# Kernel tuning notes

Hardware: AMD Instinct MI355X
Metric: run time of the kernel (lower is better)

## Reference

```python
import jax, jax.numpy as jnp
import numpy as np

B, C_IN, N = 32, 64, 128
OUT_FEATS = (64, 64, 128)
ATT_DIM = 64
EPS = 1e-5  # torch BatchNorm default


def _bn(x, g, b, m, v):
    # eval-mode BatchNorm over channel axis 1 (running stats m, v)
    shape = (1, -1) + (1,) * (x.ndim - 2)
    inv = g / jnp.sqrt(v + EPS)
    return (x - m.reshape(shape)) * inv.reshape(shape) + b.reshape(shape)


def setup_inputs() -> dict:
    key = jax.random.key(0)
    ks = iter(jax.random.split(key, 48))

    def w(shape, scale=0.05):
        return jax.random.normal(next(ks), shape, jnp.float32) * scale

    inp = {"features": jax.random.normal(next(ks), (B, C_IN, N), jnp.float32)}
    in_dims = (2 * C_IN, OUT_FEATS[0], OUT_FEATS[1])
    for li in range(3):
        o, ci = OUT_FEATS[li], in_dims[li]
        inp[f"w{li}"] = w((o, ci))                  # Conv2d 1x1, no bias (BN)
        inp[f"g{li}"] = 1.0 + w((o,))               # BN gamma
        inp[f"b{li}"] = w((o,))                     # BN beta
        inp[f"m{li}"] = w((o,))                     # BN running mean
        inp[f"v{li}"] = 1.0 + 0.1 * jax.random.uniform(next(ks), (o,), jnp.float32)
    inp["wa0"] = w((ATT_DIM, OUT_FEATS[-1]))        # attention conv (no bias)
    inp["ga"] = 1.0 + w((ATT_DIM,))
    inp["ba"] = w((ATT_DIM,))
    inp["ma"] = w((ATT_DIM,))
    inp["va"] = 1.0 + 0.1 * jax.random.uniform(next(ks), (ATT_DIM,), jnp.float32)
    inp["wa1"] = w((1, ATT_DIM))                    # final attention conv (bias)
    inp["ba1"] = w((1,))
    inp["wsc"] = w((OUT_FEATS[-1], C_IN))           # shortcut Conv1d (no bias)
    inp["gsc"] = 1.0 + w((OUT_FEATS[-1],))
    inp["bsc"] = w((OUT_FEATS[-1],))
    inp["msc"] = w((OUT_FEATS[-1],))
    inp["vsc"] = 1.0 + 0.1 * jax.random.uniform(next(ks), (OUT_FEATS[-1],), jnp.float32)
    return inp


def reference(features, w0, g0, b0, m0, v0, w1, g1, b1, m1, v1,
              w2, g2, b2, m2, v2, wa0, ga, ba, ma, va, wa1, ba1,
              wsc, gsc, bsc, msc, vsc):
    n = features.shape[-1]
    # neighbor index table: row i lists all j != i, shape (N, N-1)
    base = jnp.broadcast_to(jnp.arange(n)[None, :], (n, n))
    idx = jnp.where(base >= jnp.arange(n)[:, None], base + 1, base)[:, :-1]
    x_i = features[:, :, :, None]                   # (B,C,N,1)
    x_j = features[:, :, idx]                       # (B,C,N,N-1) gather
    x = jnp.concatenate([jnp.broadcast_to(x_i, x_j.shape), x_j - x_i], axis=1)  # (B,2C,N,N-1)
    for w_, g_, b_, m_, v_ in ((w0, g0, b0, m0, v0), (w1, g1, b1, m1, v1), (w2, g2, b2, m2, v2)):
        x = jnp.einsum('oc,bcnk->bonk', w_, x)      # 1x1 conv
        x = jax.nn.relu(_bn(x, g_, b_, m_, v_))
    # attention pooling over neighbor axis k
    a = jax.nn.relu(_bn(jnp.einsum('oc,bcnk->bonk', wa0, x), ga, ba, ma, va))
    logits = jnp.einsum('oc,bcnk->bonk', wa1, a) + ba1.reshape(1, 1, 1, 1)
    attw = jax.nn.softmax(logits[:, 0], axis=-1)    # (B,N,N-1)
    fts = jnp.einsum('bcnk,bnk->bcn', x, attw)      # (B,C_out,N)
    # shortcut branch (in_feat != out_feats[-1])
    sc = _bn(jnp.einsum('oc,bcn->bon', wsc, features), gsc, bsc, msc, vsc)
    return jax.nn.relu(sc + fts)
```

## Files before the change

kernel.cpp:

```cpp
#include <hip/hip_runtime.h>

typedef unsigned short u16;
typedef short short8 __attribute__((ext_vector_type(8)));
typedef float floatx4 __attribute__((ext_vector_type(4)));
typedef __bf16 bf16x2 __attribute__((ext_vector_type(2)));

#define MFMA16(a, b, c) __builtin_amdgcn_mfma_f32_16x16x32_bf16((a), (b), (c), 0, 0, 0)

#define W1F_OFF   0u
#define B1F_OFF   8192u
#define W2F_OFF   8448u
#define B2F_OFF   24832u
#define WA0F_OFF  25344u
#define BAF_OFF   41728u
#define WA1F_OFF  41984u
#define BA1F_OFF  42240u
#define P_OFF     42496u
#define Q_OFF     1091072u
#define SC_OFF    2139648u
#define WS_TOTAL  4236800u

__device__ __align__(256) char g_ws[WS_TOTAL];

#define LD0 72
#define LD2 136

__device__ __forceinline__ float bits2f(unsigned u) {
  union { unsigned i; float f; } v; v.i = u; return v.f;
}
__device__ __forceinline__ unsigned f2bits(float f) {
  union { float f; unsigned i; } v; v.f = f; return v.i;
}
__device__ __forceinline__ u16 f2bf(float f) {
  return (u16)((f2bits(f) + 0x8000u) >> 16);
}
__device__ __forceinline__ unsigned pack2relu(float a, float b) {
#if __has_builtin(__builtin_amdgcn_cvt_pk_bf16_f32)
  union { bf16x2 h; unsigned u; } cv;
  cv.h = __builtin_amdgcn_cvt_pk_bf16_f32(fmaxf(a, 0.f), fmaxf(b, 0.f));
  return cv.u;
#else
  unsigned lo = (f2bits(fmaxf(a, 0.f)) + 0x8000u) >> 16;
  unsigned hi = (f2bits(fmaxf(b, 0.f)) + 0x8000u) & 0xffff0000u;
  return lo | hi;
#endif
}

__global__ __launch_bounds__(256) void k_pre(
    const float* __restrict__ feat, const float* __restrict__ w0,
    const float* __restrict__ g0, const float* __restrict__ b0, const float* __restrict__ m0, const float* __restrict__ v0,
    const float* __restrict__ w1, const float* __restrict__ g1, const float* __restrict__ b1, const float* __restrict__ m1, const float* __restrict__ v1,
    const float* __restrict__ w2, const float* __restrict__ g2, const float* __restrict__ b2, const float* __restrict__ m2, const float* __restrict__ v2,
    const float* __restrict__ wa0, const float* __restrict__ ga, const float* __restrict__ ba, const float* __restrict__ ma, const float* __restrict__ va,
    const float* __restrict__ wa1, const float* __restrict__ ba1,
    const float* __restrict__ wsc, const float* __restrict__ gsc, const float* __restrict__ bsc, const float* __restrict__ msc, const float* __restrict__ vsc)
{
  __shared__ float smem[9600];
  const int t = threadIdx.x;
  char* ws = g_ws;
  const int blk = blockIdx.x;

  if (blk == 512) {
    float* fs1 = smem; float* fs2 = smem + 64; float* fsa = smem + 192;
    if (t < 64) {
      float s;
      s = g1[t] * rsqrtf(v1[t] + 1e-5f); fs1[t] = s; ((float*)(ws + B1F_OFF))[t] = b1[t] - m1[t] * s;
      s = ga[t] * rsqrtf(va[t] + 1e-5f); fsa[t] = s; ((float*)(ws + BAF_OFF))[t] = ba[t] - ma[t] * s;
      ((float*)(ws + WA1F_OFF))[t] = wa1[t];
    }
    if (t < 128) { float s = g2[t] * rsqrtf(v2[t] + 1e-5f); fs2[t] = s; ((float*)(ws + B2F_OFF))[t] = b2[t] - m2[t] * s; }
    if (t == 0) ((float*)(ws + BA1F_OFF))[0] = ba1[0];
    __syncthreads();
    u16* W1f = (u16*)(ws + W1F_OFF);
    u16* W2f = (u16*)(ws + W2F_OFF);
    u16* Wa0f = (u16*)(ws + WA0F_OFF);
    for (int i = t; i < 4096; i += 256) W1f[i]  = f2bf(fs1[i >> 6] * w1[i]);
    for (int i = t; i < 8192; i += 256) W2f[i]  = f2bf(fs2[i >> 6] * w2[i]);
    for (int i = t; i < 8192; i += 256) Wa0f[i] = f2bf(fsa[i >> 7] * wa0[i]);
    return;
  }

  const int sub = blk & 255;
  const int b = sub >> 3, n0 = (sub & 7) << 4;
  float* Xs  = smem;
  float* Wsm = smem + 1280;

  {
    const int c = t >> 2, j = (t & 3) << 2;
    *(float4*)(Xs + c * 20 + j) = *(const float4*)(feat + b * 8192 + c * 128 + n0 + j);
  }

  if (blk < 256) {
    #pragma unroll
    for (int r = 0; r < 8; r++) {
      const int i = (r * 256 + t) * 4;
      float4 v = *(const float4*)(w0 + i);
      const int o = i >> 7, c = i & 127;
      float* d = Wsm + o * 129 + c;
      d[0] = v.x; d[1] = v.y; d[2] = v.z; d[3] = v.w;
    }
    __syncthreads();
    const int o = t & 63, nb = (t >> 6) << 2;
    const float s  = g0[o] * rsqrtf(v0[o] + 1e-5f);
    const float tt = b0[o] - m0[o] * s;
    const float* wr = Wsm + o * 129;
    float dA0=0.f,dA1=0.f,dA2=0.f,dA3=0.f,dB0=0.f,dB1=0.f,dB2=0.f,dB3=0.f;
    #pragma unroll
    for (int c = 0; c < 64; c++) {
      const float a = wr[c], e = wr[64 + c];
      const float4 x = *(const float4*)(Xs + c * 20 + nb);
      dA0 += a * x.x; dA1 += a * x.y; dA2 += a * x.z; dA3 += a * x.w;
      dB0 += e * x.x; dB1 += e * x.y; dB2 += e * x.z; dB3 += e * x.w;
    }
    float* Pp = (float*)(ws + P_OFF) + (b * 128 + n0 + nb) * 64 + o;
    float* Qp = (float*)(ws + Q_OFF) + (b * 128 + n0 + nb) * 64 + o;
    Pp[0]   = s * dB0; Pp[64]  = s * dB1; Pp[128] = s * dB2; Pp[192] = s * dB3;
    Qp[0]   = s * (dA0 - dB0) + tt; Qp[64]  = s * (dA1 - dB1) + tt;
    Qp[128] = s * (dA2 - dB2) + tt; Qp[192] = s * (dA3 - dB3) + tt;
  } else {
    #pragma unroll
    for (int r = 0; r < 8; r++) {
      const int i = (r * 256 + t) * 4;
      float4 v = *(const float4*)(wsc + i);
      const int o = i >> 6, c = i & 63;
      float* d = Wsm + o * 65 + c;
      d[0] = v.x; d[1] = v.y; d[2] = v.z; d[3] = v.w;
    }
    __syncthreads();
    const int o = t & 127, h = (t >> 7) << 3;
    const float s  = gsc[o] * rsqrtf(vsc[o] + 1e-5f);
    const float tt = bsc[o] - msc[o] * s;
    const float* wr = Wsm + o * 65;
    float d0=0.f,d1=0.f,d2=0.f,d3=0.f,d4=0.f,d5=0.f,d6=0.f,d7=0.f;
    #pragma unroll
    for (int c = 0; c < 64; c++) {
      const float a = wr[c];
      const float4 x0 = *(const float4*)(Xs + c * 20 + h);
      const float4 x1 = *(const float4*)(Xs + c * 20 + h + 4);
      d0 += a * x0.x; d1 += a * x0.y; d2 += a * x0.z; d3 += a * x0.w;
      d4 += a * x1.x; d5 += a * x1.y; d6 += a * x1.z; d7 += a * x1.w;
    }
    float* SCp = (float*)(ws + SC_OFF) + (b * 128 + n0 + h) * 128 + o;
    SCp[0]   = s * d0 + tt; SCp[128] = s * d1 + tt; SCp[256] = s * d2 + tt; SCp[384] = s * d3 + tt;
    SCp[512] = s * d4 + tt; SCp[640] = s * d5 + tt; SCp[768] = s * d6 + tt; SCp[896] = s * d7 + tt;
  }
}

__global__ __launch_bounds__(256, 4) void k_main(float* __restrict__ out)
{
  __shared__ alignas(16) u16 buf[18432];
  __shared__ float parts[4][128];
  __shared__ float attws[128];

  const int blk = blockIdx.x, b = blk >> 7, n = blk & 127, t = threadIdx.x;
  const char* ws = g_ws;
  const float* Pb  = (const float*)(ws + P_OFF);
  const float* Qb  = (const float*)(ws + Q_OFF);
  const float* SCb = (const float*)(ws + SC_OFF);
  const u16*   W1f = (const u16*)(ws + W1F_OFF);
  const float* b1f = (const float*)(ws + B1F_OFF);
  const u16*   W2f = (const u16*)(ws + W2F_OFF);
  const float* b2f = (const float*)(ws + B2F_OFF);
  const u16*   Wa0f= (const u16*)(ws + WA0F_OFF);
  const float* baf = (const float*)(ws + BAF_OFF);
  const float* wa1f= (const float*)(ws + WA1F_OFF);
  const float  ba1v= *(const float*)(ws + BA1F_OFF);

  u16* H0 = buf;
  u16* H1 = buf + 9216;
  u16* H2 = buf;

  const int lane = t & 63, wid = t >> 6, quad = lane >> 4, l16 = lane & 15;
  const int koff = quad * 8;

  const short8 a1w0 = *(const short8*)(W1f + (wid * 16 + l16) * 64 + koff);
  const short8 a1w1 = *(const short8*)(W1f + (wid * 16 + l16) * 64 + 32 + koff);
  const short8 a2w00 = *(const short8*)(W2f + (wid * 32 + l16) * 64 + koff);
  const short8 a2w01 = *(const short8*)(W2f + (wid * 32 + l16) * 64 + 32 + koff);
  const short8 a2w10 = *(const short8*)(W2f + (wid * 32 + 16 + l16) * 64 + koff);
  const short8 a2w11 = *(const short8*)(W2f + (wid * 32 + 16 + l16) * 64 + 32 + koff);

  {
    const int k = t >> 1, half = t & 1;
    const int j = (k < 127) ? ((k < n) ? k : (k + 1)) : n;
    const float4* pr = (const float4*)(Pb + ((b << 7) + j) * 64 + half * 32);
    const float4* qr = (const float4*)(Qb + blk * 64 + half * 32);
    u16* dst = H0 + k * LD0 + half * 32;
    #pragma unroll
    for (int i = 0; i < 8; i++) {
      float4 p = pr[i], q = qr[i];
      uint2 sv;
      sv.x = pack2relu(q.x + p.x, q.y + p.y);
      sv.y = pack2relu(q.z + p.z, q.w + p.w);
      *(uint2*)(dst + i * 4) = sv;
    }
  }
  __syncthreads();

  {
    const int rr = wid * 16 + quad * 4;
    const float4 bb = *(const float4*)(b1f + rr);
    floatx4 binit; binit[0] = bb.x; binit[1] = bb.y; binit[2] = bb.z; binit[3] = bb.w;
    floatx4 acc[8];
    #pragma unroll
    for (int et = 0; et < 8; et++) acc[et] = binit;
    #pragma unroll
    for (int et = 0; et < 8; et++) {
      const u16* br = H0 + (et * 16 + l16) * LD0 + koff;
      short8 bf0 = *(const short8*)(br);
      short8 bf1 = *(const short8*)(br + 32);
      acc[et] = MFMA16(a1w0, bf0, acc[et]);
      acc[et] = MFMA16(a1w1, bf1, acc[et]);
    }
    #pragma unroll
    for (int et = 0; et < 8; et++) {
      uint2 sv;
      sv.x = pack2relu(acc[et][0], acc[et][1]);
      sv.y = pack2relu(acc[et][2], acc[et][3]);
      *(uint2*)(H1 + (et * 16 + l16) * LD0 + rr) = sv;
    }
  }
  __syncthreads();

  {
    const int r2 = wid * 32 + quad * 4;
    const float4 bba = *(const float4*)(b2f + r2);
    const float4 bbb = *(const float4*)(b2f + r2 + 16);
    floatx4 ia; ia[0] = bba.x; ia[1] = bba.y; ia[2] = bba.z; ia[3] = bba.w;
    floatx4 ib; ib[0] = bbb.x; ib[1] = bbb.y; ib[2] = bbb.z; ib[3] = bbb.w;
    floatx4 acc[2][8];
    #pragma unroll
    for (int et = 0; et < 8; et++) { acc[0][et] = ia; acc[1][et] = ib; }
    #pragma unroll
    for (int et = 0; et < 8; et++) {
      const u16* br = H1 + (et * 16 + l16) * LD0 + koff;
      short8 bf0 = *(const short8*)(br);
      short8 bf1 = *(const short8*)(br + 32);
      acc[0][et] = MFMA16(a2w00, bf0, acc[0][et]);
      acc[0][et] = MFMA16(a2w01, bf1, acc[0][et]);
      acc[1][et] = MFMA16(a2w10, bf0, acc[1][et]);
      acc[1][et] = MFMA16(a2w11, bf1, acc[1][et]);
    }
    __syncthreads();
    #pragma unroll
    for (int m = 0; m < 2; m++) {
      const int rr = r2 + m * 16;
      #pragma unroll
      for (int et = 0; et < 8; et++) {
        uint2 sv;
        sv.x = pack2relu(acc[m][et][0], acc[m][et][1]);
        sv.y = pack2relu(acc[m][et][2], acc[m][et][3]);
        *(uint2*)(H2 + (et * 16 + l16) * LD2 + rr) = sv;
      }
    }
  }
  __syncthreads();

  float scv = 0.f;
  if (t < 128) scv = SCb[blk * 128 + t];
  float* outp = out + ((b << 7) + (t & 127)) * 128 + n;

  {
    short8 a3[4];
    #pragma unroll
    for (int ks = 0; ks < 4; ks++)
      a3[ks] = *(const short8*)(Wa0f + (wid * 16 + l16) * 128 + ks * 32 + koff);
    const int rr = wid * 16 + quad * 4;
    const float4 bb = *(const float4*)(baf + rr);
    const float4 wv = *(const float4*)(wa1f + rr);
    floatx4 binit; binit[0] = bb.x; binit[1] = bb.y; binit[2] = bb.z; binit[3] = bb.w;
    floatx4 acc[8];
    #pragma unroll
    for (int et = 0; et < 8; et++) acc[et] = binit;
    #pragma unroll
    for (int et = 0; et < 8; et++) {
      const u16* br = H2 + (et * 16 + l16) * LD2 + koff;
      #pragma unroll
      for (int ks = 0; ks < 4; ks++) {
        short8 bf = *(const short8*)(br + ks * 32);
        acc[et] = MFMA16(a3[ks], bf, acc[et]);
      }
    }
    #pragma unroll
    for (int et = 0; et < 8; et++) {
      float p = wv.x * fmaxf(acc[et][0], 0.f) + wv.y * fmaxf(acc[et][1], 0.f)
              + wv.z * fmaxf(acc[et][2], 0.f) + wv.w * fmaxf(acc[et][3], 0.f);
      p += __shfl_xor(p, 16); p += __shfl_xor(p, 32);
      if (quad == 0) parts[wid][et * 16 + l16] = p;
    }
  }
  __syncthreads();

  if (wid == 0) {
    float a0 = parts[0][lane] + parts[1][lane] + parts[2][lane] + parts[3][lane] + ba1v;
    float a1 = (lane == 63) ? -1e30f
             : (parts[0][lane + 64] + parts[1][lane + 64] + parts[2][lane + 64] + parts[3][lane + 64] + ba1v);
    float mx = fmaxf(a0, a1);
    #pragma unroll
    for (int off = 32; off >= 1; off >>= 1) mx = fmaxf(mx, __shfl_xor(mx, off));
    float e0 = expf(a0 - mx), e1 = expf(a1 - mx);
    float sm = e0 + e1;
    #pragma unroll
    for (int off = 32; off >= 1; off >>= 1) sm += __shfl_xor(sm, off);
    float inv = 1.f / sm;
    attws[lane] = e0 * inv;
    attws[lane + 64] = e1 * inv;
  }
  __syncthreads();

  {
    const int chg = t & 15, eg = t >> 4;
    float fa[8];
    #pragma unroll
    for (int k = 0; k < 8; k++) fa[k] = 0.f;
    #pragma unroll
    for (int i = 0; i < 8; i++) {
      const int e = eg * 8 + i;
      const float w = attws[e];
      uint4 v = *(const uint4*)(H2 + e * LD2 + chg * 8);
      unsigned u;
      u = v.x; fa[0] += w * bits2f(u << 16); fa[1] += w * bits2f(u & 0xffff0000u);
      u = v.y; fa[2] += w * bits2f(u << 16); fa[3] += w * bits2f(u & 0xffff0000u);
      u = v.z; fa[4] += w * bits2f(u << 16); fa[5] += w * bits2f(u & 0xffff0000u);
      u = v.w; fa[6] += w * bits2f(u << 16); fa[7] += w * bits2f(u & 0xffff0000u);
    }
    #pragma unroll
    for (int k = 0; k < 8; k++) { fa[k] += __shfl_xor(fa[k], 16); fa[k] += __shfl_xor(fa[k], 32); }
    if (lane < 16) {
      #pragma unroll
      for (int k = 0; k < 8; k++) parts[wid][chg * 8 + k] = fa[k];
    }
  }
  __syncthreads();

  if (t < 128) {
    float fts = parts[0][t] + parts[1][t] + parts[2][t] + parts[3][t];
    *outp = fmaxf(scv + fts, 0.f);
  }
}

extern "C" void kernel_launch(void* const* d_in, const int* in_sizes, int n_in,
                              void* d_out, int out_size, void* d_ws, size_t ws_size,
                              hipStream_t stream)
{
  (void)d_ws; (void)ws_size; (void)in_sizes; (void)n_in; (void)out_size;
  const float* feat = (const float*)d_in[0];
  const float *w0 = (const float*)d_in[1],  *g0 = (const float*)d_in[2],  *b0 = (const float*)d_in[3],  *m0 = (const float*)d_in[4],  *v0 = (const float*)d_in[5];
  const float *w1 = (const float*)d_in[6],  *g1 = (const float*)d_in[7],  *b1 = (const float*)d_in[8],  *m1 = (const float*)d_in[9],  *v1 = (const float*)d_in[10];
  const float *w2 = (const float*)d_in[11], *g2 = (const float*)d_in[12], *b2 = (const float*)d_in[13], *m2 = (const float*)d_in[14], *v2 = (const float*)d_in[15];
  const float *wa0= (const float*)d_in[16], *ga = (const float*)d_in[17], *ba = (const float*)d_in[18], *ma = (const float*)d_in[19], *va = (const float*)d_in[20];
  const float *wa1= (const float*)d_in[21], *ba1= (const float*)d_in[22];
  const float *wsc= (const float*)d_in[23], *gsc= (const float*)d_in[24], *bsc= (const float*)d_in[25], *msc= (const float*)d_in[26], *vsc= (const float*)d_in[27];

  k_pre<<<dim3(513), dim3(256), 0, stream>>>(
      feat, w0, g0, b0, m0, v0, w1, g1, b1, m1, v1, w2, g2, b2, m2, v2,
      wa0, ga, ba, ma, va, wa1, ba1, wsc, gsc, bsc, msc, vsc);
  k_main<<<dim3(4096), dim3(256), 0, stream>>>((float*)d_out);
}
```

Before: 166.5 us.

## Repartition MFMA work by neighbor rows per wave and build layer-0 operands in registers

Layer 0 no longer goes through shared memory. Each wave now builds its bf16 B-fragments for 32 neighbor rows directly from P+Q in registers and feeds the layer-1 MFMA with them, which removes the H0 store and one barrier. Layer 2 uses a 2x2 split over channel and neighbor halves. The attention layer assigns neighbor rows to waves, so the logit partials no longer need a cross-wave reduction. The cost is that weight fragments are reloaded per m-tile inside loops rather than held in registers, which raises global/L1 weight traffic and may change register pressure.

```diff
diff --git a/kernel.cpp b/kernel.cpp
--- a/kernel.cpp
+++ b/kernel.cpp
@@ -166,93 +166,95 @@
   const float* wa1f= (const float*)(ws + WA1F_OFF);
   const float  ba1v= *(const float*)(ws + BA1F_OFF);
 
-  u16* H0 = buf;
   u16* H1 = buf + 9216;
   u16* H2 = buf;
 
   const int lane = t & 63, wid = t >> 6, quad = lane >> 4, l16 = lane & 15;
   const int koff = quad * 8;
 
-  const short8 a1w0 = *(const short8*)(W1f + (wid * 16 + l16) * 64 + koff);
-  const short8 a1w1 = *(const short8*)(W1f + (wid * 16 + l16) * 64 + 32 + koff);
-  const short8 a2w00 = *(const short8*)(W2f + (wid * 32 + l16) * 64 + koff);
-  const short8 a2w01 = *(const short8*)(W2f + (wid * 32 + l16) * 64 + 32 + koff);
-  const short8 a2w10 = *(const short8*)(W2f + (wid * 32 + 16 + l16) * 64 + koff);
-  const short8 a2w11 = *(const short8*)(W2f + (wid * 32 + 16 + l16) * 64 + 32 + koff);
-
-  {
-    const int k = t >> 1, half = t & 1;
-    const int j = (k < 127) ? ((k < n) ? k : (k + 1)) : n;
-    const float4* pr = (const float4*)(Pb + ((b << 7) + j) * 64 + half * 32);
-    const float4* qr = (const float4*)(Qb + blk * 64 + half * 32);
-    u16* dst = H0 + k * LD0 + half * 32;
-    #pragma unroll
-    for (int i = 0; i < 8; i++) {
-      float4 p = pr[i], q = qr[i];
-      uint2 sv;
-      sv.x = pack2relu(q.x + p.x, q.y + p.y);
-      sv.y = pack2relu(q.z + p.z, q.w + p.w);
-      *(uint2*)(dst + i * 4) = sv;
-    }
-  }
-  __syncthreads();
-
-  {
-    const int rr = wid * 16 + quad * 4;
-    const float4 bb = *(const float4*)(b1f + rr);
-    floatx4 binit; binit[0] = bb.x; binit[1] = bb.y; binit[2] = bb.z; binit[3] = bb.w;
-    floatx4 acc[8];
-    #pragma unroll
-    for (int et = 0; et < 8; et++) acc[et] = binit;
-    #pragma unroll
-    for (int et = 0; et < 8; et++) {
-      const u16* br = H0 + (et * 16 + l16) * LD0 + koff;
-      short8 bf0 = *(const short8*)(br);
-      short8 bf1 = *(const short8*)(br + 32);
-      acc[et] = MFMA16(a1w0, bf0, acc[et]);
-      acc[et] = MFMA16(a1w1, bf1, acc[et]);
-    }
-    #pragma unroll
-    for (int et = 0; et < 8; et++) {
-      uint2 sv;
-      sv.x = pack2relu(acc[et][0], acc[et][1]);
-      sv.y = pack2relu(acc[et][2], acc[et][3]);
-      *(uint2*)(H1 + (et * 16 + l16) * LD0 + rr) = sv;
-    }
-  }
-  __syncthreads();
-
-  {
-    const int r2 = wid * 32 + quad * 4;
-    const float4 bba = *(const float4*)(b2f + r2);
-    const float4 bbb = *(const float4*)(b2f + r2 + 16);
-    floatx4 ia; ia[0] = bba.x; ia[1] = bba.y; ia[2] = bba.z; ia[3] = bba.w;
-    floatx4 ib; ib[0] = bbb.x; ib[1] = bbb.y; ib[2] = bbb.z; ib[3] = bbb.w;
-    floatx4 acc[2][8];
-    #pragma unroll
-    for (int et = 0; et < 8; et++) { acc[0][et] = ia; acc[1][et] = ib; }
-    #pragma unroll
-    for (int et = 0; et < 8; et++) {
-      const u16* br = H1 + (et * 16 + l16) * LD0 + koff;
-      short8 bf0 = *(const short8*)(br);
-      short8 bf1 = *(const short8*)(br + 32);
-      acc[0][et] = MFMA16(a2w00, bf0, acc[0][et]);
-      acc[0][et] = MFMA16(a2w01, bf1, acc[0][et]);
-      acc[1][et] = MFMA16(a2w10, bf0, acc[1][et]);
-      acc[1][et] = MFMA16(a2w11, bf1, acc[1][et]);
+  {
+    const float* Qr = Qb + blk * 64;
+    const float4 q0a = *(const float4*)(Qr + koff);
+    const float4 q0b = *(const float4*)(Qr + koff + 4);
+    const float4 q1a = *(const float4*)(Qr + 32 + koff);
+    const float4 q1b = *(const float4*)(Qr + 32 + koff + 4);
+    short8 bfr[2][2];
+    #pragma unroll
+    for (int et2 = 0; et2 < 2; et2++) {
+      const int e = wid * 32 + et2 * 16 + l16;
+      const int j = (e < 127) ? ((e < n) ? e : (e + 1)) : n;
+      const float* Pr = Pb + (((b << 7) + j) << 6);
+      const float4 p0a = *(const float4*)(Pr + koff);
+      const float4 p0b = *(const float4*)(Pr + koff + 4);
+      const float4 p1a = *(const float4*)(Pr + 32 + koff);
+      const float4 p1b = *(const float4*)(Pr + 32 + koff + 4);
+      union { short8 s; uint4 u; } c0, c1;
+      c0.u.x = pack2relu(q0a.x + p0a.x, q0a.y + p0a.y);
+      c0.u.y = pack2relu(q0a.z + p0a.z, q0a.w + p0a.w);
+      c0.u.z = pack2relu(q0b.x + p0b.x, q0b.y + p0b.y);
+      c0.u.w = pack2relu(q0b.z + p0b.z, q0b.w + p0b.w);
+      c1.u.x = pack2relu(q1a.x + p1a.x, q1a.y + p1a.y);
+      c1.u.y = pack2relu(q1a.z + p1a.z, q1a.w + p1a.w);
+      c1.u.z = pack2relu(q1b.x + p1b.x, q1b.y + p1b.y);
+      c1.u.w = pack2relu(q1b.z + p1b.z, q1b.w + p1b.w);
+      bfr[et2][0] = c0.s; bfr[et2][1] = c1.s;
+    }
+    uint2 sv[4][2];
+    #pragma unroll
+    for (int mt = 0; mt < 4; mt++) {
+      const float4 bb = *(const float4*)(b1f + mt * 16 + quad * 4);
+      floatx4 binit; binit[0] = bb.x; binit[1] = bb.y; binit[2] = bb.z; binit[3] = bb.w;
+      const short8 a0 = *(const short8*)(W1f + (mt * 16 + l16) * 64 + koff);
+      const short8 a1 = *(const short8*)(W1f + (mt * 16 + l16) * 64 + 32 + koff);
+      #pragma unroll
+      for (int et2 = 0; et2 < 2; et2++) {
+        floatx4 a = binit;
+        a = MFMA16(a0, bfr[et2][0], a);
+        a = MFMA16(a1, bfr[et2][1], a);
+        sv[mt][et2].x = pack2relu(a[0], a[1]);
+        sv[mt][et2].y = pack2relu(a[2], a[3]);
+      }
+    }
+    #pragma unroll
+    for (int mt = 0; mt < 4; mt++)
+      #pragma unroll
+      for (int et2 = 0; et2 < 2; et2++)
+        *(uint2*)(H1 + (wid * 32 + et2 * 16 + l16) * LD0 + mt * 16 + quad * 4) = sv[mt][et2];
+  }
+  __syncthreads();
+
+  {
+    const int wc = wid >> 1, we = wid & 1;
+    short8 bfr[4][2];
+    #pragma unroll
+    for (int et2 = 0; et2 < 4; et2++) {
+      const u16* br = H1 + (we * 64 + et2 * 16 + l16) * LD0 + koff;
+      bfr[et2][0] = *(const short8*)(br);
+      bfr[et2][1] = *(const short8*)(br + 32);
+    }
+    uint2 sv[4][4];
+    #pragma unroll
+    for (int mt = 0; mt < 4; mt++) {
+      const int chb = wc * 64 + mt * 16;
+      const float4 bb = *(const float4*)(b2f + chb + quad * 4);
+      floatx4 binit; binit[0] = bb.x; binit[1] = bb.y; binit[2] = bb.z; binit[3] = bb.w;
+      const short8 a0 = *(const short8*)(W2f + (chb + l16) * 64 + koff);
+      const short8 a1 = *(const short8*)(W2f + (chb + l16) * 64 + 32 + koff);
+      #pragma unroll
+      for (int et2 = 0; et2 < 4; et2++) {
+        floatx4 a = binit;
+        a = MFMA16(a0, bfr[et2][0], a);
+        a = MFMA16(a1, bfr[et2][1], a);
+        sv[mt][et2].x = pack2relu(a[0], a[1]);
+        sv[mt][et2].y = pack2relu(a[2], a[3]);
+      }
     }
     __syncthreads();
     #pragma unroll
-    for (int m = 0; m < 2; m++) {
-      const int rr = r2 + m * 16;
-      #pragma unroll
-      for (int et = 0; et < 8; et++) {
-        uint2 sv;
-        sv.x = pack2relu(acc[m][et][0], acc[m][et][1]);
-        sv.y = pack2relu(acc[m][et][2], acc[m][et][3]);
-        *(uint2*)(H2 + (et * 16 + l16) * LD2 + rr) = sv;
-      }
-    }
+    for (int mt = 0; mt < 4; mt++)
+      #pragma unroll
+      for (int et2 = 0; et2 < 4; et2++)
+        *(uint2*)(H2 + (we * 64 + et2 * 16 + l16) * LD2 + wc * 64 + mt * 16 + quad * 4) = sv[mt][et2];
   }
   __syncthreads();
 
@@ -261,40 +263,44 @@
   float* outp = out + ((b << 7) + (t & 127)) * 128 + n;
 
   {
-    short8 a3[4];
-    #pragma unroll
-    for (int ks = 0; ks < 4; ks++)
-      a3[ks] = *(const short8*)(Wa0f + (wid * 16 + l16) * 128 + ks * 32 + koff);
-    const int rr = wid * 16 + quad * 4;
-    const float4 bb = *(const float4*)(baf + rr);
-    const float4 wv = *(const float4*)(wa1f + rr);
-    floatx4 binit; binit[0] = bb.x; binit[1] = bb.y; binit[2] = bb.z; binit[3] = bb.w;
-    floatx4 acc[8];
-    #pragma unroll
-    for (int et = 0; et < 8; et++) acc[et] = binit;
-    #pragma unroll
-    for (int et = 0; et < 8; et++) {
-      const u16* br = H2 + (et * 16 + l16) * LD2 + koff;
+    short8 bfr[2][4];
+    #pragma unroll
+    for (int et2 = 0; et2 < 2; et2++) {
+      const u16* br = H2 + (wid * 32 + et2 * 16 + l16) * LD2 + koff;
+      #pragma unroll
+      for (int ks = 0; ks < 4; ks++)
+        bfr[et2][ks] = *(const short8*)(br + ks * 32);
+    }
+    float p0 = 0.f, p1 = 0.f;
+    #pragma unroll
+    for (int mt = 0; mt < 4; mt++) {
+      const float4 bb = *(const float4*)(baf + mt * 16 + quad * 4);
+      const float4 wv = *(const float4*)(wa1f + mt * 16 + quad * 4);
+      floatx4 binit; binit[0] = bb.x; binit[1] = bb.y; binit[2] = bb.z; binit[3] = bb.w;
+      floatx4 ac0 = binit, ac1 = binit;
       #pragma unroll
       for (int ks = 0; ks < 4; ks++) {
-        short8 bf = *(const short8*)(br + ks * 32);
-        acc[et] = MFMA16(a3[ks], bf, acc[et]);
+        const short8 aa = *(const short8*)(Wa0f + (mt * 16 + l16) * 128 + ks * 32 + koff);
+        ac0 = MFMA16(aa, bfr[0][ks], ac0);
+        ac1 = MFMA16(aa, bfr[1][ks], ac1);
       }
-    }
-    #pragma unroll
-    for (int et = 0; et < 8; et++) {
-      float p = wv.x * fmaxf(acc[et][0], 0.f) + wv.y * fmaxf(acc[et][1], 0.f)
-              + wv.z * fmaxf(acc[et][2], 0.f) + wv.w * fmaxf(acc[et][3], 0.f);
-      p += __shfl_xor(p, 16); p += __shfl_xor(p, 32);
-      if (quad == 0) parts[wid][et * 16 + l16] = p;
+      p0 += wv.x * fmaxf(ac0[0], 0.f) + wv.y * fmaxf(ac0[1], 0.f)
+          + wv.z * fmaxf(ac0[2], 0.f) + wv.w * fmaxf(ac0[3], 0.f);
+      p1 += wv.x * fmaxf(ac1[0], 0.f) + wv.y * fmaxf(ac1[1], 0.f)
+          + wv.z * fmaxf(ac1[2], 0.f) + wv.w * fmaxf(ac1[3], 0.f);
+    }
+    p0 += __shfl_xor(p0, 16); p0 += __shfl_xor(p0, 32);
+    p1 += __shfl_xor(p1, 16); p1 += __shfl_xor(p1, 32);
+    if (quad == 0) {
+      parts[0][wid * 32 + l16]      = p0;
+      parts[0][wid * 32 + 16 + l16] = p1;
     }
   }
   __syncthreads();
 
   if (wid == 0) {
-    float a0 = parts[0][lane] + parts[1][lane] + parts[2][lane] + parts[3][lane] + ba1v;
-    float a1 = (lane == 63) ? -1e30f
-             : (parts[0][lane + 64] + parts[1][lane + 64] + parts[2][lane + 64] + parts[3][lane + 64] + ba1v);
+    float a0 = parts[0][lane] + ba1v;
+    float a1 = (lane == 63) ? -1e30f : (parts[0][lane + 64] + ba1v);
     float mx = fmaxf(a0, a1);
     #pragma unroll
     for (int off = 32; off >= 1; off >>= 1) mx = fmaxf(mx, __shfl_xor(mx, off));
```

Result: slower. 199.1 us (+19.6%).

## Swizzle LDS activation tiles and hoist weight and H2 loads before barriers

Applied to the files above, without the earlier changes.

Replaces padded LDS row strides (72/136) with XOR-swizzled unpadded layouts for the H0/H1/H2 activation tiles, which shrinks shared memory use and aims to avoid bank conflicts on the MFMA operand reads. The H0 fill now writes 16-byte chunks instead of 8-byte ones. The Wa0 weight fragment loads are moved ahead of a barrier, and the H2 rows used for attention pooling are read into registers before the softmax barrier, so memory latency overlaps with synchronisation. Holding the H2 rows in registers raises register pressure, which may affect occupancy at 4 blocks per CU.

```diff
diff --git a/kernel.cpp b/kernel.cpp
--- a/kernel.cpp
+++ b/kernel.cpp
@@ -22,9 +22,6 @@
 
 __device__ __align__(256) char g_ws[WS_TOTAL];
 
-#define LD0 72
-#define LD2 136
-
 __device__ __forceinline__ float bits2f(unsigned u) {
   union { unsigned i; float f; } v; v.i = u; return v.f;
 }
@@ -44,6 +41,13 @@
   unsigned hi = (f2bits(fmaxf(b, 0.f)) + 0x8000u) & 0xffff0000u;
   return lo | hi;
 #endif
+}
+
+__device__ __forceinline__ int sw64(int row, int col) {
+  return (row << 6) + ((((col >> 3) ^ (row & 7)) << 3) | (col & 7));
+}
+__device__ __forceinline__ int sw128(int row, int col) {
+  return (row << 7) + ((((col >> 3) ^ (row & 7)) << 3) | (col & 7));
 }
 
 __global__ __launch_bounds__(256) void k_pre(
@@ -148,7 +152,7 @@
 
 __global__ __launch_bounds__(256, 4) void k_main(float* __restrict__ out)
 {
-  __shared__ alignas(16) u16 buf[18432];
+  __shared__ alignas(16) u16 buf[16384];
   __shared__ float parts[4][128];
   __shared__ float attws[128];
 
@@ -167,7 +171,7 @@
   const float  ba1v= *(const float*)(ws + BA1F_OFF);
 
   u16* H0 = buf;
-  u16* H1 = buf + 9216;
+  u16* H1 = buf + 8192;
   u16* H2 = buf;
 
   const int lane = t & 63, wid = t >> 6, quad = lane >> 4, l16 = lane & 15;
@@ -185,14 +189,16 @@
     const int j = (k < 127) ? ((k < n) ? k : (k + 1)) : n;
     const float4* pr = (const float4*)(Pb + ((b << 7) + j) * 64 + half * 32);
     const float4* qr = (const float4*)(Qb + blk * 64 + half * 32);
-    u16* dst = H0 + k * LD0 + half * 32;
-    #pragma unroll
-    for (int i = 0; i < 8; i++) {
-      float4 p = pr[i], q = qr[i];
-      uint2 sv;
-      sv.x = pack2relu(q.x + p.x, q.y + p.y);
-      sv.y = pack2relu(q.z + p.z, q.w + p.w);
-      *(uint2*)(dst + i * 4) = sv;
+    #pragma unroll
+    for (int ii = 0; ii < 4; ii++) {
+      float4 p0 = pr[2 * ii],     q0 = qr[2 * ii];
+      float4 p1 = pr[2 * ii + 1], q1 = qr[2 * ii + 1];
+      uint4 sv;
+      sv.x = pack2relu(q0.x + p0.x, q0.y + p0.y);
+      sv.y = pack2relu(q0.z + p0.z, q0.w + p0.w);
+      sv.z = pack2relu(q1.x + p1.x, q1.y + p1.y);
+      sv.w = pack2relu(q1.z + p1.z, q1.w + p1.w);
+      *(uint4*)(H0 + sw64(k, half * 32 + ii * 8)) = sv;
     }
   }
   __syncthreads();
@@ -206,9 +212,9 @@
     for (int et = 0; et < 8; et++) acc[et] = binit;
     #pragma unroll
     for (int et = 0; et < 8; et++) {
-      const u16* br = H0 + (et * 16 + l16) * LD0 + koff;
-      short8 bf0 = *(const short8*)(br);
-      short8 bf1 = *(const short8*)(br + 32);
+      const int row = et * 16 + l16;
+      short8 bf0 = *(const short8*)(H0 + sw64(row, koff));
+      short8 bf1 = *(const short8*)(H0 + sw64(row, koff + 32));
       acc[et] = MFMA16(a1w0, bf0, acc[et]);
       acc[et] = MFMA16(a1w1, bf1, acc[et]);
     }
@@ -217,7 +223,7 @@
       uint2 sv;
       sv.x = pack2relu(acc[et][0], acc[et][1]);
       sv.y = pack2relu(acc[et][2], acc[et][3]);
-      *(uint2*)(H1 + (et * 16 + l16) * LD0 + rr) = sv;
+      *(uint2*)(H1 + sw64(et * 16 + l16, rr)) = sv;
     }
   }
   __syncthreads();
@@ -233,9 +239,9 @@
     for (int et = 0; et < 8; et++) { acc[0][et] = ia; acc[1][et] = ib; }
     #pragma unroll
     for (int et = 0; et < 8; et++) {
-      const u16* br = H1 + (et * 16 + l16) * LD0 + koff;
-      short8 bf0 = *(const short8*)(br);
-      short8 bf1 = *(const short8*)(br + 32);
+      const int row = et * 16 + l16;
+      short8 bf0 = *(const short8*)(H1 + sw64(row, koff));
+      short8 bf1 = *(const short8*)(H1 + sw64(row, koff + 32));
       acc[0][et] = MFMA16(a2w00, bf0, acc[0][et]);
       acc[0][et] = MFMA16(a2w01, bf1, acc[0][et]);
       acc[1][et] = MFMA16(a2w10, bf0, acc[1][et]);
@@ -250,10 +256,16 @@
         uint2 sv;
         sv.x = pack2relu(acc[m][et][0], acc[m][et][1]);
         sv.y = pack2relu(acc[m][et][2], acc[m][et][3]);
-        *(uint2*)(H2 + (et * 16 + l16) * LD2 + rr) = sv;
+        *(uint2*)(H2 + sw128(et * 16 + l16, rr)) = sv;
       }
     }
   }
+
+  short8 a3[4];
+  #pragma unroll
+  for (int ks = 0; ks < 4; ks++)
+    a3[ks] = *(const short8*)(Wa0f + (wid * 16 + l16) * 128 + ks * 32 + koff);
+
   __syncthreads();
 
   float scv = 0.f;
@@ -261,10 +273,6 @@
   float* outp = out + ((b << 7) + (t & 127)) * 128 + n;
 
   {
-    short8 a3[4];
-    #pragma unroll
-    for (int ks = 0; ks < 4; ks++)
-      a3[ks] = *(const short8*)(Wa0f + (wid * 16 + l16) * 128 + ks * 32 + koff);
     const int rr = wid * 16 + quad * 4;
     const float4 bb = *(const float4*)(baf + rr);
     const float4 wv = *(const float4*)(wa1f + rr);
@@ -274,10 +282,10 @@
     for (int et = 0; et < 8; et++) acc[et] = binit;
     #pragma unroll
     for (int et = 0; et < 8; et++) {
-      const u16* br = H2 + (et * 16 + l16) * LD2 + koff;
+      const int row = et * 16 + l16;
       #pragma unroll
       for (int ks = 0; ks < 4; ks++) {
-        short8 bf = *(const short8*)(br + ks * 32);
+        short8 bf = *(const short8*)(H2 + sw128(row, koff + ks * 32));
         acc[et] = MFMA16(a3[ks], bf, acc[et]);
       }
     }
@@ -289,6 +297,13 @@
       if (quad == 0) parts[wid][et * 16 + l16] = p;
     }
   }
+
+  const int chg = t & 15, eg = t >> 4;
+  uint4 hv[8];
+  #pragma unroll
+  for (int i = 0; i < 8; i++)
+    hv[i] = *(const uint4*)(H2 + sw128(eg * 8 + i, chg * 8));
+
   __syncthreads();
 
   if (wid == 0) {
@@ -309,15 +324,13 @@
   __syncthreads();
 
   {
-    const int chg = t & 15, eg = t >> 4;
     float fa[8];
     #pragma unroll
     for (int k = 0; k < 8; k++) fa[k] = 0.f;
     #pragma unroll
     for (int i = 0; i < 8; i++) {
-      const int e = eg * 8 + i;
-      const float w = attws[e];
-      uint4 v = *(const uint4*)(H2 + e * LD2 + chg * 8);
+      const float w = attws[eg * 8 + i];
+      uint4 v = hv[i];
       unsigned u;
       u = v.x; fa[0] += w * bits2f(u << 16); fa[1] += w * bits2f(u & 0xffff0000u);
       u = v.y; fa[2] += w * bits2f(u << 16); fa[3] += w * bits2f(u & 0xffff0000u);
```

After: 168.5 us. About the same (+1.2%).
